# Performance work log

Measured on AMD Instinct MI355X. Metric: run time of the kernel, lower is better.

The kernel has to match this reference:

```python
import jax, jax.numpy as jnp
import numpy as np

NUM_TOPICS = 100
VOCAB = 8192
MC_N = 20
MD_N = 20
LAMBDA_D = 0.7
LAMBDA_A = 100.0
WARMUP_RATIO = 0.5
NUM_EPOCHS = 200


def setup_inputs() -> dict:
    key = jax.random.key(0)
    k1, k2 = jax.random.split(key)
    beta = jax.random.normal(k1, (NUM_TOPICS, VOCAB), dtype=jnp.float32)
    W = jax.random.uniform(k2, (VOCAB, VOCAB), dtype=jnp.float32)
    # fill_diagonal_(1) in __init__
    d = jnp.arange(VOCAB)
    W = W.at[d, d].set(1.0)
    return {"beta": beta, "coherence_weight": W, "epoch": 120}


def reference(beta, coherence_weight, epoch):
    K, V = beta.shape
    rows = jnp.arange(K)[:, None]

    # --- Mc: top-Mc_n mask -> additive -99999 on non-topk entries ---
    _, mc_idx = jax.lax.top_k(beta, MC_N)                      # [K, Mc_n]
    Mc = jnp.zeros_like(beta).at[rows, mc_idx].set(1.0)        # [K, V]
    Mc_add = (1.0 - Mc) * (-99999.0)

    # softmax over masked beta is detached in the original
    p = jax.lax.stop_gradient(jax.nn.softmax(beta + Mc_add, axis=1))
    M = p @ coherence_weight                                    # [K, V]

    # row-wise min-max normalize, then Wc = 1 - normalized
    m_min = jnp.min(M, axis=1, keepdims=True)
    m_max = jnp.max(M, axis=1, keepdims=True)
    Wc = 1.0 - (M - m_min) / (m_max - m_min)

    loss = 100.0 * jax.nn.softmax(beta, axis=1) ** 2 * Wc       # [K, V]

    # --- diversity mask Md (lambda_d > 0.5 branch) ---
    _, md_idx = jax.lax.top_k(beta, MD_N)
    Md_mask = jnp.zeros_like(beta).at[rows, md_idx].set(1.0)    # [K, V]
    # Md[t, v] = any other row has v in its top-Md_n
    col_sum = jnp.sum(Md_mask, axis=0)                          # [V]
    Md = (col_sum[None, :] - Md_mask) > 0                       # [K, V] bool

    pos = jnp.sum(jnp.where(Md, loss, 0.0))
    neg = jnp.sum(jnp.where(Md, 0.0, loss))
    total = (pos * LAMBDA_D + neg * (1.0 - LAMBDA_D)) * 2.0

    warmup_epochs = int(WARMUP_RATIO * NUM_EPOCHS)              # 100
    lambda_a_delta = LAMBDA_A / warmup_epochs
    lambda_a = epoch * lambda_a_delta if epoch < warmup_epochs else LAMBDA_A
    return lambda_a * total
```

## Files before the change

### kernel.cpp

```cpp
#include <hip/hip_runtime.h>
#include <math.h>

#define NT 100
#define VOCAB 8192
#define TOPN 20
#define HALVES 2
#define HCOLS 4096
#define NB (NT * HALVES)
#define CAP 4096

__global__ __launch_bounds__(1024) void topk_kernel(
    const float* __restrict__ beta,
    int*   __restrict__ top_idx,
    float* __restrict__ top_p,
    float* __restrict__ rowstats)
{
    const int k = blockIdx.x;
    const int t = threadIdx.x;

    __shared__ float sred[16];
    __shared__ int   sredi[16];
    __shared__ int   s_base;
    __shared__ float cu[CAP];
    __shared__ unsigned short ci[CAP];
    __shared__ float s_winv[TOPN];
    __shared__ int   s_wini[TOPN];
    __shared__ float s_ps;

    const float* row = beta + (size_t)k * VOCAB;

    float4 r0 = *reinterpret_cast<const float4*>(row + (size_t)t * 4);
    float4 r1 = *reinterpret_cast<const float4*>(row + (size_t)(1024 + t) * 4);

    float mx = fmaxf(fmaxf(fmaxf(r0.x, r0.y), fmaxf(r0.z, r0.w)),
                     fmaxf(fmaxf(r1.x, r1.y), fmaxf(r1.z, r1.w)));
#pragma unroll
    for (int off = 32; off >= 1; off >>= 1) mx = fmaxf(mx, __shfl_down(mx, off));
    if ((t & 63) == 0) sred[t >> 6] = mx;
    __syncthreads();
    float rowmax = sred[0];
#pragma unroll
    for (int w = 1; w < 16; ++w) rowmax = fmaxf(rowmax, sred[w]);
    __syncthreads();

    float T = rowmax - 2.0f;
    for (int guard = 0; guard < 64; ++guard) {
        int c = 0;
        c += (r0.x >= T) + (r0.y >= T) + (r0.z >= T) + (r0.w >= T);
        c += (r1.x >= T) + (r1.y >= T) + (r1.z >= T) + (r1.w >= T);
#pragma unroll
        for (int off = 32; off >= 1; off >>= 1) c += __shfl_down(c, off);
        if ((t & 63) == 0) sredi[t >> 6] = c;
        __syncthreads();
        int cnt = 0;
#pragma unroll
        for (int w = 0; w < 16; ++w) cnt += sredi[w];
        if (cnt >= TOPN) break;
        T -= 0.5f;
        __syncthreads();
    }
    if (t == 0) s_base = 0;
    __syncthreads();

#pragma unroll
    for (int i = 0; i < 2; ++i) {
        const float4 rr = (i == 0) ? r0 : r1;
#pragma unroll
        for (int e = 0; e < 4; ++e) {
            const float v = (&rr.x)[e];
            const int idx = (i * 1024 + t) * 4 + e;
            const bool pr = (v >= T);
            const unsigned long long mask = __ballot(pr);
            const int lane = t & 63;
            const int pre = __popcll(mask & ((1ull << lane) - 1ull));
            int base = 0;
            if (lane == 0) base = atomicAdd(&s_base, __popcll(mask));
            base = __shfl(base, 0);
            if (pr) {
                const int p = base + pre;
                if (p < CAP) { cu[p] = v; ci[p] = (unsigned short)idx; }
            }
        }
    }
    __syncthreads();
    const int ncand = min(s_base, CAP);

    if (t < 64) {
        for (int it = 0; it < TOPN; ++it) {
            float bv = -INFINITY; int bp = -1;
            for (int p = t; p < ncand; p += 64) {
                const float v = cu[p];
                if (v > bv) { bv = v; bp = p; }
            }
#pragma unroll
            for (int off = 32; off >= 1; off >>= 1) {
                const float ov = __shfl_down(bv, off);
                const int   op = __shfl_down(bp, off);
                if (ov > bv) { bv = ov; bp = op; }
            }
            bp = __shfl(bp, 0);
            bv = __shfl(bv, 0);
            if (t == 0) { s_winv[it] = bv; s_wini[it] = ci[bp]; }
            cu[bp] = -INFINITY;
        }
    }
    __syncthreads();

    if (t == 0) {
        float ps = 0.f;
#pragma unroll
        for (int j = 0; j < TOPN; ++j) ps += expf(s_winv[j] - rowmax);
        s_ps = ps;
    }
    __syncthreads();
    if (t < TOPN) {
        top_idx[k * TOPN + t] = s_wini[t];
        top_p[k * TOPN + t]   = expf(s_winv[t] - rowmax) / s_ps;
    }

    float se = expf(r0.x - rowmax) + expf(r0.y - rowmax)
             + expf(r0.z - rowmax) + expf(r0.w - rowmax)
             + expf(r1.x - rowmax) + expf(r1.y - rowmax)
             + expf(r1.z - rowmax) + expf(r1.w - rowmax);
#pragma unroll
    for (int off = 32; off >= 1; off >>= 1) se += __shfl_down(se, off);
    if ((t & 63) == 0) sred[t >> 6] = se;
    __syncthreads();
    if (t == 0) {
        float s = 0.f;
#pragma unroll
        for (int w = 0; w < 16; ++w) s += sred[w];
        rowstats[2 * k + 0] = rowmax;
        rowstats[2 * k + 1] = s;
    }
}

__global__ __launch_bounds__(1024) void fused_kernel(
    const float* __restrict__ beta,
    const float* __restrict__ W,
    const int*   __restrict__ top_idx,
    const float* __restrict__ top_p,
    const float* __restrict__ rowstats,
    float* __restrict__ part6)
{
    const int b = blockIdx.x;
    const int k = b >> 1;
    const int h = b & 1;
    const int t = threadIdx.x;

    __shared__ int   sIdx[TOPN];
    __shared__ float sP[TOPN];
    __shared__ int   cnt[HCOLS];
    __shared__ float sA[16], sB[16], sC[16], sD[16], sE[16], sF[16];

    if (t < TOPN) { sIdx[t] = top_idx[k * TOPN + t]; sP[t] = top_p[k * TOPN + t]; }
#pragma unroll
    for (int i = 0; i < HCOLS / 1024; ++i) cnt[i * 1024 + t] = 0;
    __syncthreads();

    const int lo = h * HCOLS;
    for (int e = t; e < NT * TOPN; e += 1024) {
        const int v = top_idx[e] - lo;
        if ((unsigned)v < (unsigned)HCOLS) atomicAdd(&cnt[v], 1);
    }
    if (t < TOPN) {
        const int v = sIdx[t] - lo;
        if ((unsigned)v < (unsigned)HCOLS) atomicSub(&cnt[v], 1);
    }

    int   idx_r[TOPN];
    float p_r[TOPN];
#pragma unroll
    for (int j = 0; j < TOPN; ++j) { idx_r[j] = sIdx[j]; p_r[j] = sP[j]; }

    const int col = lo + t * 4;
    float4 m = make_float4(0.f, 0.f, 0.f, 0.f);
#pragma unroll
    for (int j = 0; j < TOPN; ++j) {
        const float4 w = *reinterpret_cast<const float4*>(W + (size_t)idx_r[j] * VOCAB + col);
        const float pj = p_r[j];
        m.x += pj * w.x; m.y += pj * w.y; m.z += pj * w.z; m.w += pj * w.w;
    }

    float mn  = fminf(fminf(m.x, m.y), fminf(m.z, m.w));
    float mxv = fmaxf(fmaxf(m.x, m.y), fmaxf(m.z, m.w));

    const float rmax = rowstats[2 * k + 0];
    const float rinv = 1.0f / rowstats[2 * k + 1];
    const float4 bv = *reinterpret_cast<const float4*>(beta + (size_t)k * VOCAB + col);
    float4 w4;
    w4.x = expf(bv.x - rmax) * rinv;  w4.x = 100.f * w4.x * w4.x;
    w4.y = expf(bv.y - rmax) * rinv;  w4.y = 100.f * w4.y * w4.y;
    w4.z = expf(bv.z - rmax) * rinv;  w4.z = 100.f * w4.z * w4.z;
    w4.w = expf(bv.w - rmax) * rinv;  w4.w = 100.f * w4.w * w4.w;

    __syncthreads();

    float Apos = 0.f, Bpos = 0.f, Aneg = 0.f, Bneg = 0.f;
    {
        const int lc = t * 4;
        if (cnt[lc + 0] > 0) { Apos += w4.x; Bpos += w4.x * m.x; } else { Aneg += w4.x; Bneg += w4.x * m.x; }
        if (cnt[lc + 1] > 0) { Apos += w4.y; Bpos += w4.y * m.y; } else { Aneg += w4.y; Bneg += w4.y * m.y; }
        if (cnt[lc + 2] > 0) { Apos += w4.z; Bpos += w4.z * m.z; } else { Aneg += w4.z; Bneg += w4.z * m.z; }
        if (cnt[lc + 3] > 0) { Apos += w4.w; Bpos += w4.w * m.w; } else { Aneg += w4.w; Bneg += w4.w * m.w; }
    }

#pragma unroll
    for (int off = 32; off >= 1; off >>= 1) {
        mn   = fminf(mn,  __shfl_down(mn,  off));
        mxv  = fmaxf(mxv, __shfl_down(mxv, off));
        Apos += __shfl_down(Apos, off);
        Bpos += __shfl_down(Bpos, off);
        Aneg += __shfl_down(Aneg, off);
        Bneg += __shfl_down(Bneg, off);
    }
    if ((t & 63) == 0) {
        const int w = t >> 6;
        sA[w] = mn; sB[w] = mxv; sC[w] = Apos; sD[w] = Bpos; sE[w] = Aneg; sF[w] = Bneg;
    }
    __syncthreads();
    if (t == 0) {
        float a = sA[0], bb = sB[0], cc = 0.f, dd = 0.f, ee = 0.f, ff = 0.f;
#pragma unroll
        for (int w = 0; w < 16; ++w) {
            a  = fminf(a,  sA[w]);
            bb = fmaxf(bb, sB[w]);
            cc += sC[w]; dd += sD[w]; ee += sE[w]; ff += sF[w];
        }
        part6[b * 6 + 0] = a;
        part6[b * 6 + 1] = bb;
        part6[b * 6 + 2] = cc;
        part6[b * 6 + 3] = dd;
        part6[b * 6 + 4] = ee;
        part6[b * 6 + 5] = ff;
    }
}

__global__ __launch_bounds__(128) void finalize_kernel(
    const float* __restrict__ part6,
    const int*   __restrict__ epoch,
    float* __restrict__ out)
{
    const int t = threadIdx.x;
    __shared__ float sp[128], sn[128];
    float pos = 0.f, neg = 0.f;
    if (t < NT) {
        float mn = INFINITY, mxv = -INFINITY;
        float Ap = 0.f, Bp = 0.f, An = 0.f, Bn = 0.f;
        for (int h = 0; h < HALVES; ++h) {
            const float* p6 = part6 + (size_t)(t * HALVES + h) * 6;
            mn  = fminf(mn,  p6[0]);
            mxv = fmaxf(mxv, p6[1]);
            Ap += p6[2]; Bp += p6[3]; An += p6[4]; Bn += p6[5];
        }
        const float inv = 1.0f / (mxv - mn);
        pos = Ap - inv * (Bp - mn * Ap);
        neg = An - inv * (Bn - mn * An);
    }
    sp[t] = pos; sn[t] = neg;
    __syncthreads();
    if (t == 0) {
        float P = 0.f, N = 0.f;
        for (int i = 0; i < NT; ++i) { P += sp[i]; N += sn[i]; }
        const float total = (P * 0.7f + N * 0.3f) * 2.0f;
        const int e = *epoch;
        const float la = (e < 100) ? (float)e : 100.0f;
        *out = la * total;
    }
}

extern "C" void kernel_launch(void* const* d_in, const int* in_sizes, int n_in,
                              void* d_out, int out_size, void* d_ws, size_t ws_size,
                              hipStream_t stream)
{
    (void)in_sizes; (void)n_in; (void)out_size; (void)ws_size;
    const float* beta  = (const float*)d_in[0];
    const float* W     = (const float*)d_in[1];
    const int*   epoch = (const int*)d_in[2];
    float* out = (float*)d_out;

    char* ws = (char*)d_ws;
    int*   top_idx  = (int*)ws;    ws += NT * TOPN * sizeof(int);
    float* top_p    = (float*)ws;  ws += NT * TOPN * sizeof(float);
    float* rowstats = (float*)ws;  ws += NT * 2 * sizeof(float);
    float* part6    = (float*)ws;  ws += NB * 6 * sizeof(float);

    topk_kernel<<<NT, 1024, 0, stream>>>(beta, top_idx, top_p, rowstats);
    fused_kernel<<<NB, 1024, 0, stream>>>(beta, W, top_idx, top_p, rowstats, part6);
    finalize_kernel<<<1, 128, 0, stream>>>(part6, epoch, out);
}
```

Before: 51.14 us.

## Split fused kernel into smaller column chunks and prefetch W rows before histogram

Each topic row is now split into 8 chunks of 1024 columns, handled by 256-thread blocks, instead of 2 halves of 4096 columns with 1024-thread blocks. This gives 800 small blocks instead of 200 large ones, to spread work across the compute units. All 20 gathered W float4 loads and the beta load are issued up front, before the shared-memory histogram of other topics' top-k indices is built, so their memory latency overlaps the atomics. In exchange, each block repeats the 2000-entry histogram scan (four times as many blocks scan it), and holding 20 float4 values per thread raises register pressure.

```diff
diff --git a/kernel.cpp b/kernel.cpp
--- a/kernel.cpp
+++ b/kernel.cpp
@@ -4,9 +4,9 @@
 #define NT 100
 #define VOCAB 8192
 #define TOPN 20
-#define HALVES 2
-#define HCOLS 4096
-#define NB (NT * HALVES)
+#define CHUNKS 8
+#define CCOLS 1024
+#define NB (NT * CHUNKS)
 #define CAP 4096
 
 __global__ __launch_bounds__(1024) void topk_kernel(
@@ -135,7 +135,7 @@
     }
 }
 
-__global__ __launch_bounds__(1024) void fused_kernel(
+__global__ __launch_bounds__(256) void fused_kernel(
     const float* __restrict__ beta,
     const float* __restrict__ W,
     const int*   __restrict__ top_idx,
@@ -144,42 +144,50 @@
     float* __restrict__ part6)
 {
     const int b = blockIdx.x;
-    const int k = b >> 1;
-    const int h = b & 1;
+    const int k = b / CHUNKS;
+    const int c = b % CHUNKS;
     const int t = threadIdx.x;
 
     __shared__ int   sIdx[TOPN];
     __shared__ float sP[TOPN];
-    __shared__ int   cnt[HCOLS];
-    __shared__ float sA[16], sB[16], sC[16], sD[16], sE[16], sF[16];
+    __shared__ int   cnt[CCOLS];
+    __shared__ float sA[4], sB[4], sC[4], sD[4], sE[4], sF[4];
 
     if (t < TOPN) { sIdx[t] = top_idx[k * TOPN + t]; sP[t] = top_p[k * TOPN + t]; }
 #pragma unroll
-    for (int i = 0; i < HCOLS / 1024; ++i) cnt[i * 1024 + t] = 0;
-    __syncthreads();
-
-    const int lo = h * HCOLS;
-    for (int e = t; e < NT * TOPN; e += 1024) {
+    for (int i = 0; i < CCOLS / 256; ++i) cnt[i * 256 + t] = 0;
+    __syncthreads();
+
+    int   idx_r[TOPN];
+    float p_r[TOPN];
+#pragma unroll
+    for (int j = 0; j < TOPN; ++j) { idx_r[j] = sIdx[j]; p_r[j] = sP[j]; }
+
+    const int lo  = c * CCOLS;
+    const int col = lo + t * 4;
+    float4 w_r[TOPN];
+#pragma unroll
+    for (int j = 0; j < TOPN; ++j)
+        w_r[j] = *reinterpret_cast<const float4*>(W + (size_t)idx_r[j] * VOCAB + col);
+    const float4 bv = *reinterpret_cast<const float4*>(beta + (size_t)k * VOCAB + col);
+
+#pragma unroll 8
+    for (int e = t; e < NT * TOPN; e += 256) {
         const int v = top_idx[e] - lo;
-        if ((unsigned)v < (unsigned)HCOLS) atomicAdd(&cnt[v], 1);
-    }
+        if ((unsigned)v < (unsigned)CCOLS) atomicAdd(&cnt[v], 1);
+    }
+    __syncthreads();
     if (t < TOPN) {
         const int v = sIdx[t] - lo;
-        if ((unsigned)v < (unsigned)HCOLS) atomicSub(&cnt[v], 1);
-    }
-
-    int   idx_r[TOPN];
-    float p_r[TOPN];
-#pragma unroll
-    for (int j = 0; j < TOPN; ++j) { idx_r[j] = sIdx[j]; p_r[j] = sP[j]; }
-
-    const int col = lo + t * 4;
+        if ((unsigned)v < (unsigned)CCOLS) atomicSub(&cnt[v], 1);
+    }
+
     float4 m = make_float4(0.f, 0.f, 0.f, 0.f);
 #pragma unroll
     for (int j = 0; j < TOPN; ++j) {
-        const float4 w = *reinterpret_cast<const float4*>(W + (size_t)idx_r[j] * VOCAB + col);
         const float pj = p_r[j];
-        m.x += pj * w.x; m.y += pj * w.y; m.z += pj * w.z; m.w += pj * w.w;
+        m.x += pj * w_r[j].x; m.y += pj * w_r[j].y;
+        m.z += pj * w_r[j].z; m.w += pj * w_r[j].w;
     }
 
     float mn  = fminf(fminf(m.x, m.y), fminf(m.z, m.w));
@@ -187,7 +195,6 @@
 
     const float rmax = rowstats[2 * k + 0];
     const float rinv = 1.0f / rowstats[2 * k + 1];
-    const float4 bv = *reinterpret_cast<const float4*>(beta + (size_t)k * VOCAB + col);
     float4 w4;
     w4.x = expf(bv.x - rmax) * rinv;  w4.x = 100.f * w4.x * w4.x;
     w4.y = expf(bv.y - rmax) * rinv;  w4.y = 100.f * w4.y * w4.y;
@@ -220,19 +227,12 @@
     }
     __syncthreads();
     if (t == 0) {
-        float a = sA[0], bb = sB[0], cc = 0.f, dd = 0.f, ee = 0.f, ff = 0.f;
-#pragma unroll
-        for (int w = 0; w < 16; ++w) {
-            a  = fminf(a,  sA[w]);
-            bb = fmaxf(bb, sB[w]);
-            cc += sC[w]; dd += sD[w]; ee += sE[w]; ff += sF[w];
-        }
-        part6[b * 6 + 0] = a;
-        part6[b * 6 + 1] = bb;
-        part6[b * 6 + 2] = cc;
-        part6[b * 6 + 3] = dd;
-        part6[b * 6 + 4] = ee;
-        part6[b * 6 + 5] = ff;
+        part6[b * 6 + 0] = fminf(fminf(sA[0], sA[1]), fminf(sA[2], sA[3]));
+        part6[b * 6 + 1] = fmaxf(fmaxf(sB[0], sB[1]), fmaxf(sB[2], sB[3]));
+        part6[b * 6 + 2] = sC[0] + sC[1] + sC[2] + sC[3];
+        part6[b * 6 + 3] = sD[0] + sD[1] + sD[2] + sD[3];
+        part6[b * 6 + 4] = sE[0] + sE[1] + sE[2] + sE[3];
+        part6[b * 6 + 5] = sF[0] + sF[1] + sF[2] + sF[3];
     }
 }
 
@@ -247,8 +247,8 @@
     if (t < NT) {
         float mn = INFINITY, mxv = -INFINITY;
         float Ap = 0.f, Bp = 0.f, An = 0.f, Bn = 0.f;
-        for (int h = 0; h < HALVES; ++h) {
-            const float* p6 = part6 + (size_t)(t * HALVES + h) * 6;
+        for (int cc = 0; cc < CHUNKS; ++cc) {
+            const float* p6 = part6 + (size_t)(t * CHUNKS + cc) * 6;
             mn  = fminf(mn,  p6[0]);
             mxv = fmaxf(mxv, p6[1]);
             Ap += p6[2]; Bp += p6[3]; An += p6[4]; Bn += p6[5];
@@ -286,6 +286,6 @@
     float* part6    = (float*)ws;  ws += NB * 6 * sizeof(float);
 
     topk_kernel<<<NT, 1024, 0, stream>>>(beta, top_idx, top_p, rowstats);
-    fused_kernel<<<NB, 1024, 0, stream>>>(beta, W, top_idx, top_p, rowstats, part6);
+    fused_kernel<<<NB, 256, 0, stream>>>(beta, W, top_idx, top_p, rowstats, part6);
     finalize_kernel<<<1, 128, 0, stream>>>(part6, epoch, out);
 }
```

New measurement: 50.87 us. About the same (-0.5%).

## Fold finalize into fused kernel via atomicAdd, one 512-thread block per row

Applied to the files above, without the earlier changes.

Removes the separate finalize kernel launch. The output is zeroed in topk_kernel, and each block of the fused kernel combines its row's normalization terms and atomically adds its contribution to the output. The fused kernel now uses one 512-thread block per topic that loops over four column slices with a full-vocabulary count histogram, instead of two 1024-thread blocks per row. This saves a launch and the partial-buffer round trip, but halves the grid to 100 blocks, which may reduce parallelism on a GPU with many CUs and makes the float summation order nondeterministic.

```diff
diff --git a/kernel.cpp b/kernel.cpp
--- a/kernel.cpp
+++ b/kernel.cpp
@@ -4,19 +4,18 @@
 #define NT 100
 #define VOCAB 8192
 #define TOPN 20
-#define HALVES 2
-#define HCOLS 4096
-#define NB (NT * HALVES)
 #define CAP 4096
 
 __global__ __launch_bounds__(1024) void topk_kernel(
     const float* __restrict__ beta,
     int*   __restrict__ top_idx,
     float* __restrict__ top_p,
-    float* __restrict__ rowstats)
+    float* __restrict__ rowstats,
+    float* __restrict__ out)
 {
     const int k = blockIdx.x;
     const int t = threadIdx.x;
+    if (k == 0 && t == 0) *out = 0.f;
 
     __shared__ float sred[16];
     __shared__ int   sredi[16];
@@ -135,74 +134,71 @@
     }
 }
 
-__global__ __launch_bounds__(1024) void fused_kernel(
+__global__ __launch_bounds__(512) void fused_kernel(
     const float* __restrict__ beta,
     const float* __restrict__ W,
     const int*   __restrict__ top_idx,
     const float* __restrict__ top_p,
     const float* __restrict__ rowstats,
-    float* __restrict__ part6)
+    const int*   __restrict__ epoch,
+    float* __restrict__ out)
 {
-    const int b = blockIdx.x;
-    const int k = b >> 1;
-    const int h = b & 1;
+    const int k = blockIdx.x;
     const int t = threadIdx.x;
 
+    __shared__ int   cnt[VOCAB];
     __shared__ int   sIdx[TOPN];
     __shared__ float sP[TOPN];
-    __shared__ int   cnt[HCOLS];
-    __shared__ float sA[16], sB[16], sC[16], sD[16], sE[16], sF[16];
+    __shared__ float sA[8], sB[8], sC[8], sD[8], sE[8], sF[8];
 
     if (t < TOPN) { sIdx[t] = top_idx[k * TOPN + t]; sP[t] = top_p[k * TOPN + t]; }
 #pragma unroll
-    for (int i = 0; i < HCOLS / 1024; ++i) cnt[i * 1024 + t] = 0;
-    __syncthreads();
-
-    const int lo = h * HCOLS;
-    for (int e = t; e < NT * TOPN; e += 1024) {
-        const int v = top_idx[e] - lo;
-        if ((unsigned)v < (unsigned)HCOLS) atomicAdd(&cnt[v], 1);
-    }
-    if (t < TOPN) {
-        const int v = sIdx[t] - lo;
-        if ((unsigned)v < (unsigned)HCOLS) atomicSub(&cnt[v], 1);
-    }
+    for (int i = 0; i < VOCAB / 512; ++i) cnt[i * 512 + t] = 0;
+    __syncthreads();
+
+#pragma unroll 4
+    for (int e = t; e < NT * TOPN; e += 512) atomicAdd(&cnt[top_idx[e]], 1);
+    if (t < TOPN) atomicSub(&cnt[sIdx[t]], 1);
 
     int   idx_r[TOPN];
     float p_r[TOPN];
 #pragma unroll
     for (int j = 0; j < TOPN; ++j) { idx_r[j] = sIdx[j]; p_r[j] = sP[j]; }
 
-    const int col = lo + t * 4;
-    float4 m = make_float4(0.f, 0.f, 0.f, 0.f);
-#pragma unroll
-    for (int j = 0; j < TOPN; ++j) {
-        const float4 w = *reinterpret_cast<const float4*>(W + (size_t)idx_r[j] * VOCAB + col);
-        const float pj = p_r[j];
-        m.x += pj * w.x; m.y += pj * w.y; m.z += pj * w.z; m.w += pj * w.w;
-    }
-
-    float mn  = fminf(fminf(m.x, m.y), fminf(m.z, m.w));
-    float mxv = fmaxf(fmaxf(m.x, m.y), fmaxf(m.z, m.w));
-
     const float rmax = rowstats[2 * k + 0];
     const float rinv = 1.0f / rowstats[2 * k + 1];
-    const float4 bv = *reinterpret_cast<const float4*>(beta + (size_t)k * VOCAB + col);
-    float4 w4;
-    w4.x = expf(bv.x - rmax) * rinv;  w4.x = 100.f * w4.x * w4.x;
-    w4.y = expf(bv.y - rmax) * rinv;  w4.y = 100.f * w4.y * w4.y;
-    w4.z = expf(bv.z - rmax) * rinv;  w4.z = 100.f * w4.z * w4.z;
-    w4.w = expf(bv.w - rmax) * rinv;  w4.w = 100.f * w4.w * w4.w;
-
-    __syncthreads();
-
+
+    __syncthreads();
+
+    float mn = INFINITY, mxv = -INFINITY;
     float Apos = 0.f, Bpos = 0.f, Aneg = 0.f, Bneg = 0.f;
-    {
-        const int lc = t * 4;
-        if (cnt[lc + 0] > 0) { Apos += w4.x; Bpos += w4.x * m.x; } else { Aneg += w4.x; Bneg += w4.x * m.x; }
-        if (cnt[lc + 1] > 0) { Apos += w4.y; Bpos += w4.y * m.y; } else { Aneg += w4.y; Bneg += w4.y * m.y; }
-        if (cnt[lc + 2] > 0) { Apos += w4.z; Bpos += w4.z * m.z; } else { Aneg += w4.z; Bneg += w4.z * m.z; }
-        if (cnt[lc + 3] > 0) { Apos += w4.w; Bpos += w4.w * m.w; } else { Aneg += w4.w; Bneg += w4.w * m.w; }
+
+#pragma unroll
+    for (int s = 0; s < 4; ++s) {
+        const int col = s * 2048 + t * 4;
+
+        float4 m = make_float4(0.f, 0.f, 0.f, 0.f);
+#pragma unroll
+        for (int j = 0; j < TOPN; ++j) {
+            const float4 w = *reinterpret_cast<const float4*>(W + (size_t)idx_r[j] * VOCAB + col);
+            const float pj = p_r[j];
+            m.x += pj * w.x; m.y += pj * w.y; m.z += pj * w.z; m.w += pj * w.w;
+        }
+        mn  = fminf(mn,  fminf(fminf(m.x, m.y), fminf(m.z, m.w)));
+        mxv = fmaxf(mxv, fmaxf(fmaxf(m.x, m.y), fmaxf(m.z, m.w)));
+
+        const float4 bv = *reinterpret_cast<const float4*>(beta + (size_t)k * VOCAB + col);
+        float4 w4;
+        w4.x = expf(bv.x - rmax) * rinv;  w4.x = 100.f * w4.x * w4.x;
+        w4.y = expf(bv.y - rmax) * rinv;  w4.y = 100.f * w4.y * w4.y;
+        w4.z = expf(bv.z - rmax) * rinv;  w4.z = 100.f * w4.z * w4.z;
+        w4.w = expf(bv.w - rmax) * rinv;  w4.w = 100.f * w4.w * w4.w;
+
+        const int4 c4 = *reinterpret_cast<const int4*>(cnt + col);
+        if (c4.x > 0) { Apos += w4.x; Bpos += w4.x * m.x; } else { Aneg += w4.x; Bneg += w4.x * m.x; }
+        if (c4.y > 0) { Apos += w4.y; Bpos += w4.y * m.y; } else { Aneg += w4.y; Bneg += w4.y * m.y; }
+        if (c4.z > 0) { Apos += w4.z; Bpos += w4.z * m.z; } else { Aneg += w4.z; Bneg += w4.z * m.z; }
+        if (c4.w > 0) { Apos += w4.w; Bpos += w4.w * m.w; } else { Aneg += w4.w; Bneg += w4.w * m.w; }
     }
 
 #pragma unroll
@@ -220,52 +216,19 @@
     }
     __syncthreads();
     if (t == 0) {
-        float a = sA[0], bb = sB[0], cc = 0.f, dd = 0.f, ee = 0.f, ff = 0.f;
-#pragma unroll
-        for (int w = 0; w < 16; ++w) {
-            a  = fminf(a,  sA[w]);
-            bb = fmaxf(bb, sB[w]);
-            cc += sC[w]; dd += sD[w]; ee += sE[w]; ff += sF[w];
-        }
-        part6[b * 6 + 0] = a;
-        part6[b * 6 + 1] = bb;
-        part6[b * 6 + 2] = cc;
-        part6[b * 6 + 3] = dd;
-        part6[b * 6 + 4] = ee;
-        part6[b * 6 + 5] = ff;
-    }
-}
-
-__global__ __launch_bounds__(128) void finalize_kernel(
-    const float* __restrict__ part6,
-    const int*   __restrict__ epoch,
-    float* __restrict__ out)
-{
-    const int t = threadIdx.x;
-    __shared__ float sp[128], sn[128];
-    float pos = 0.f, neg = 0.f;
-    if (t < NT) {
-        float mn = INFINITY, mxv = -INFINITY;
-        float Ap = 0.f, Bp = 0.f, An = 0.f, Bn = 0.f;
-        for (int h = 0; h < HALVES; ++h) {
-            const float* p6 = part6 + (size_t)(t * HALVES + h) * 6;
-            mn  = fminf(mn,  p6[0]);
-            mxv = fmaxf(mxv, p6[1]);
-            Ap += p6[2]; Bp += p6[3]; An += p6[4]; Bn += p6[5];
-        }
-        const float inv = 1.0f / (mxv - mn);
-        pos = Ap - inv * (Bp - mn * Ap);
-        neg = An - inv * (Bn - mn * An);
-    }
-    sp[t] = pos; sn[t] = neg;
-    __syncthreads();
-    if (t == 0) {
-        float P = 0.f, N = 0.f;
-        for (int i = 0; i < NT; ++i) { P += sp[i]; N += sn[i]; }
-        const float total = (P * 0.7f + N * 0.3f) * 2.0f;
+        float a = sA[0], b = sB[0], Ap = 0.f, Bp = 0.f, An = 0.f, Bn = 0.f;
+#pragma unroll
+        for (int w = 0; w < 8; ++w) {
+            a  = fminf(a, sA[w]);
+            b  = fmaxf(b, sB[w]);
+            Ap += sC[w]; Bp += sD[w]; An += sE[w]; Bn += sF[w];
+        }
+        const float inv = 1.0f / (b - a);
+        const float pos = Ap - inv * (Bp - a * Ap);
+        const float neg = An - inv * (Bn - a * An);
         const int e = *epoch;
         const float la = (e < 100) ? (float)e : 100.0f;
-        *out = la * total;
+        atomicAdd(out, la * (pos * 0.7f + neg * 0.3f) * 2.0f);
     }
 }
 
@@ -283,9 +246,7 @@
     int*   top_idx  = (int*)ws;    ws += NT * TOPN * sizeof(int);
     float* top_p    = (float*)ws;  ws += NT * TOPN * sizeof(float);
     float* rowstats = (float*)ws;  ws += NT * 2 * sizeof(float);
-    float* part6    = (float*)ws;  ws += NB * 6 * sizeof(float);
-
-    topk_kernel<<<NT, 1024, 0, stream>>>(beta, top_idx, top_p, rowstats);
-    fused_kernel<<<NB, 1024, 0, stream>>>(beta, W, top_idx, top_p, rowstats, part6);
-    finalize_kernel<<<1, 128, 0, stream>>>(part6, epoch, out);
+
+    topk_kernel<<<NT, 1024, 0, stream>>>(beta, top_idx, top_p, rowstats, out);
+    fused_kernel<<<NT, 512, 0, stream>>>(beta, W, top_idx, top_p, rowstats, epoch, out);
 }
```

After: 53.55 us. 1.05x slower.
